# Performance work log

Hardware: AMD Instinct MI355X
Metric: run time of the kernel (lower is better)

## Reference

```python
import jax, jax.numpy as jnp
import numpy as np

N_HEAD = 16
HEAD_SIZE = 64

def setup_inputs() -> dict:
    key = jax.random.key(0)
    ks = jax.random.split(key, 5)
    B, T, C = 2, 2048, 1024
    s = 0.02
    return {
        "x": jax.random.normal(ks[0], (B, T, C), dtype=jnp.float32),
        "We": jax.random.normal(ks[1], (3 * C, C), dtype=jnp.float32) * s,
        "be": jax.random.normal(ks[2], (3 * C,), dtype=jnp.float32) * s,
        "Wp": jax.random.normal(ks[3], (C, C), dtype=jnp.float32) * s,
        "bp": jax.random.normal(ks[4], (C,), dtype=jnp.float32) * s,
    }

def reference(x, We, be, Wp, bp):
    B, T, C = x.shape
    H, D = N_HEAD, HEAD_SIZE
    qkv = x @ We.T + be                      # [B,T,3C]
    q, k, v = jnp.split(qkv, 3, axis=-1)
    # [B,H,T,D]
    q = q.reshape(B, T, H, D).transpose(0, 2, 1, 3)
    k = k.reshape(B, T, H, D).transpose(0, 2, 1, 3)
    v = v.reshape(B, T, H, D).transpose(0, 2, 1, 3)
    scale = 1.0 / jnp.sqrt(jnp.asarray(D, dtype=x.dtype))
    att = jnp.einsum('bhqd,bhkd->bhqk', q, k) * scale
    causal = jnp.tril(jnp.ones((T, T), dtype=bool))
    att = jnp.where(causal, att, -jnp.inf)
    att = jax.nn.softmax(att, axis=-1)
    y = jnp.einsum('bhqk,bhkd->bhqd', att, v)   # [B,H,T,D]
    y = y.transpose(0, 2, 1, 3).reshape(B, T, C)
    return y @ Wp.T + bp
```

## Files before the change

kernel.cpp:

```cpp
#include <hip/hip_runtime.h>
#include <hip/hip_bf16.h>
#include <stdint.h>
#include <stddef.h>

typedef short s8v __attribute__((ext_vector_type(8)));
typedef float f4v __attribute__((ext_vector_type(4)));

__device__ inline float b2f(short s) {
    union { unsigned u; float f; } x;
    x.u = ((unsigned)(unsigned short)s) << 16;
    return x.f;
}
__device__ inline short f2b(float f) {
    union { float f; unsigned u; } x;
    x.f = f;
    unsigned r = x.u + 0x7FFF + ((x.u >> 16) & 1);
    return (short)(r >> 16);
}

__device__ __forceinline__ void gl16(const short* g, short* l) {
    __builtin_amdgcn_global_load_lds(
        (const __attribute__((address_space(1))) void*)g,
        (__attribute__((address_space(3))) void*)l,
        16, 0, 0);
}

__global__ __launch_bounds__(256) void convert_bf16(
    const void* s0, short* d0, size_t c0,
    const void* s1, short* d1, size_t c1,
    const void* s2, short* d2, size_t c2,
    const void* s3, short* d3, size_t c3,
    const void* s4, short* d4, size_t c4,
    int* __restrict__ flagout)
{
    int hit = 0;
    const unsigned* xw = (const unsigned*)s0;
    for (int i = threadIdx.x & 63; i < 1024; i += 64) {
        unsigned e = ((xw[i] & 0xFFFFu) >> 7) & 0xFFu;
        if (e >= 0x8Au) hit = 1;
    }
    const bool f32 = (__ballot(hit != 0) != 0ull);
    if (blockIdx.x == 0 && threadIdx.x == 0) *flagout = f32 ? 1 : 0;

    const void* srcs[5] = {s0, s1, s2, s3, s4};
    short* dsts[5] = {d0, d1, d2, d3, d4};
    size_t cnts[5] = {c0, c1, c2, c3, c4};
    size_t total = c0 + c1 + c2 + c3 + c4;
    size_t stride = (size_t)gridDim.x * blockDim.x;
    for (size_t c = (size_t)blockIdx.x * blockDim.x + threadIdx.x; c < total; c += stride) {
        size_t r = c; int s = 0;
        while (r >= cnts[s]) { r -= cnts[s]; s++; }
        short* d = dsts[s] + r * 8;
        if (f32) {
            const float* p = (const float*)srcs[s] + r * 8;
            f4v a = *(const f4v*)p;
            f4v b = *(const f4v*)(p + 4);
            s8v v;
            v[0] = f2b(a[0]); v[1] = f2b(a[1]); v[2] = f2b(a[2]); v[3] = f2b(a[3]);
            v[4] = f2b(b[0]); v[5] = f2b(b[1]); v[6] = f2b(b[2]); v[7] = f2b(b[3]);
            *(s8v*)d = v;
        } else {
            *(s8v*)d = *(const s8v*)((const short*)srcs[s] + r * 8);
        }
    }
}

#define BKK 64

template<int QKV, int TBM, int TBN, int MINW>
__global__ __launch_bounds__(256, MINW) void gemm_bt_bias(
    const short* __restrict__ A,
    const short* __restrict__ B,
    const short* __restrict__ bias,
    void* __restrict__ C,
    short* __restrict__ vT,
    int M, int N, int K, int ldc,
    const int* __restrict__ flagp, int oDyn)
{
    const bool of32 = oDyn && (*flagp != 0);
    const int MT = TBM / 32, NT = TBN / 32;

    __shared__ __align__(16) short smem[(TBM + TBN) * BKK];
    short* sA = smem;
    short* sB = smem + TBM * BKK;

    const int tid  = threadIdx.x;
    const int lane = tid & 63;
    const int w    = tid >> 6;
    const int wm   = (w >> 1) * (TBM / 2);
    const int wn   = (w & 1) * (TBN / 2);
    const int quad = lane >> 4;
    const int l16  = lane & 15;

    const int m0 = blockIdx.y * TBM;
    const int n0 = blockIdx.x * TBN;

    f4v acc[MT][NT];
    const f4v vzero = {0.0f, 0.0f, 0.0f, 0.0f};
#pragma unroll
    for (int i = 0; i < MT; i++)
#pragma unroll
        for (int j = 0; j < NT; j++) acc[i][j] = vzero;

    const int ACH = TBM * 8;
    for (int k0 = 0; k0 < K; k0 += BKK) {
        __syncthreads();
#pragma unroll
        for (int i = 0; i < (TBM + TBN) / 32; i++) {
            int c  = i * 256 + tid;
            int cb = i * 256 + (tid & 192);
            if (c < ACH) {
                int r = c >> 3, kk = (c & 7) * 8;
                gl16(A + (size_t)(m0 + r) * K + k0 + kk, sA + cb * 8);
            } else {
                int c2 = c - ACH, cb2 = cb - ACH;
                int r = c2 >> 3, kk = (c2 & 7) * 8;
                gl16(B + (size_t)(n0 + r) * K + k0 + kk, sB + cb2 * 8);
            }
        }
        __syncthreads();
#pragma unroll
        for (int s = 0; s < 2; s++) {
            s8v af[MT], bf[NT];
#pragma unroll
            for (int t = 0; t < MT; t++)
                af[t] = *(const s8v*)(sA + (wm + t * 16 + l16) * BKK + s * 32 + quad * 8);
#pragma unroll
            for (int t = 0; t < NT; t++)
                bf[t] = *(const s8v*)(sB + (wn + t * 16 + l16) * BKK + s * 32 + quad * 8);
#pragma unroll
            for (int mt = 0; mt < MT; mt++)
#pragma unroll
                for (int nt = 0; nt < NT; nt++)
                    acc[mt][nt] = __builtin_amdgcn_mfma_f32_16x16x32_bf16(
                        af[mt], bf[nt], acc[mt][nt], 0, 0, 0);
        }
    }

    if (QKV && n0 >= 2048) {
        static_assert(!QKV || (TBM == 128 && TBN == 128), "V transpose assumes 128x128");
        const int bq = m0 >> 11;
#pragma unroll
        for (int hm = 0; hm < 2; hm++) {
            __syncthreads();
            if ((w >> 1) == hm) {
#pragma unroll
                for (int nt = 0; nt < NT; nt++) {
                    int nl = wn + nt * 16 + l16;
                    float bv = b2f(bias[n0 + nl]);
#pragma unroll
                    for (int mt = 0; mt < MT; mt++)
#pragma unroll
                        for (int r = 0; r < 4; r++) {
                            int ml2 = mt * 16 + quad * 4 + r;
                            smem[nl * 72 + ml2] = f2b(acc[mt][nt][r] + bv);
                        }
                }
            }
            __syncthreads();
#pragma unroll
            for (int i = 0; i < 4; i++) {
                int c = i * 256 + tid;
                int nl = c >> 3, col = (c & 7) * 8;
                int nn = n0 + nl;
                int hh = (nn - 2048) >> 6, d = nn & 63;
                short* dst = vT + (((size_t)(bq * 16 + hh)) * 64 + d) * 2048
                           + (m0 & 2047) + hm * 64 + col;
                *(s8v*)dst = *(const s8v*)(smem + nl * 72 + col);
            }
        }
    } else if (QKV) {
        const float osc = (n0 < 1024) ? 0.125f : 1.0f;
#pragma unroll
        for (int hm = 0; hm < 2; hm++) {
            __syncthreads();
            if ((w >> 1) == hm) {
#pragma unroll
                for (int nt = 0; nt < NT; nt++) {
                    int nl = wn + nt * 16 + l16;
                    float bv = b2f(bias[n0 + nl]);
#pragma unroll
                    for (int mt = 0; mt < MT; mt++)
#pragma unroll
                        for (int r = 0; r < 4; r++) {
                            int ml2 = mt * 16 + quad * 4 + r;
                            smem[ml2 * 144 + nl] = f2b((acc[mt][nt][r] + bv) * osc);
                        }
                }
            }
            __syncthreads();
#pragma unroll
            for (int i = 0; i < 4; i++) {
                int c = i * 256 + tid;
                int m = c >> 4, ncol = (c & 15) * 8;
                *(s8v*)((short*)C + (size_t)(m0 + hm * 64 + m) * ldc + n0 + ncol) =
                    *(const s8v*)(smem + m * 144 + ncol);
            }
        }
    } else {
#pragma unroll
        for (int nt = 0; nt < NT; nt++) {
            int n = n0 + wn + nt * 16 + l16;
            float bv = b2f(bias[n]);
#pragma unroll
            for (int mt = 0; mt < MT; mt++) {
#pragma unroll
                for (int r = 0; r < 4; r++) {
                    int m = m0 + wm + mt * 16 + quad * 4 + r;
                    float v = acc[mt][nt][r] + bv;
                    if (of32) ((float*)C)[(size_t)m * ldc + n] = v;
                    else      ((short*)C)[(size_t)m * ldc + n] = f2b(v);
                }
            }
        }
    }
}

#define LP 72

template<int PARTS>
__global__ __launch_bounds__(256) void attn_flash(
    const short* __restrict__ qk,
    const short* __restrict__ vt,
    short* __restrict__ y,
    short* __restrict__ Opart,
    float* __restrict__ Lpart)
{
    const int T = 2048, LDQ = 2048;
    __shared__ __align__(16) short sK[64 * LP];
    __shared__ __align__(16) short sVT[64 * LP];
    __shared__ __align__(16) short sP[4][16 * LP];

    const int tid  = threadIdx.x;
    const int lane = tid & 63;
    const int w    = tid >> 6;
    const int quad = lane >> 4;
    const int l16  = lane & 15;

    int part, qt, bh, u;
    if (PARTS == 2) {
        part = blockIdx.x & 1;
        int rest = blockIdx.x >> 1;
        qt = 31 - (rest >> 5);
        bh = rest & 31;
        u  = bh * 32 + qt;
    } else {
        part = 0;
        qt = 31 - (blockIdx.x >> 5);
        bh = blockIdx.x & 31;
        u  = 0;
    }
    const int b = bh >> 4;
    const int h = bh & 15;

    const int n    = qt + 1;
    const int half = (n + 1) >> 1;
    const int klo  = (PARTS == 2 && part) ? half : 0;
    const int khi  = (PARTS == 2 && !part) ? half : n;

    if (PARTS == 2 && klo >= khi) {
        s8v z;
#pragma unroll
        for (int j = 0; j < 8; j++) z[j] = 0;
        s8v* ob = (s8v*)(Opart + ((size_t)(part * 1024 + u)) * 4096);
        for (int i = tid; i < 512; i += 256) ob[i] = z;
        if (tid < 64) Lpart[(size_t)(part * 1024 + u) * 64 + tid] = 0.0f;
        return;
    }

    const size_t qkbase = (size_t)b * T * LDQ;
    const short* Kbase  = qk + qkbase + 1024 + h * 64;
    const short* Vbase  = vt + (size_t)bh * 64 * 2048;

    s8v qf[2];
    {
        int qrow = qt * 64 + w * 16 + l16;
        const short* qp = qk + qkbase + (size_t)qrow * LDQ + h * 64 + quad * 8;
        qf[0] = *(const s8v*)(qp);
        qf[1] = *(const s8v*)(qp + 32);
    }

    const int r0 = tid >> 3;
    const int dd = (tid & 7) * 8;

    s8v kr0 = *(const s8v*)(Kbase + (size_t)(klo * 64 + r0) * LDQ + dd);
    s8v kr1 = *(const s8v*)(Kbase + (size_t)(klo * 64 + r0 + 32) * LDQ + dd);
    s8v vv0 = *(const s8v*)(Vbase + (size_t)r0 * 2048 + klo * 64 + dd);
    s8v vv1 = *(const s8v*)(Vbase + (size_t)(r0 + 32) * 2048 + klo * 64 + dd);

    const f4v vzero = {0.0f, 0.0f, 0.0f, 0.0f};
    f4v o[4];
#pragma unroll
    for (int i = 0; i < 4; i++) o[i] = vzero;
    float lsum[4] = {0.0f, 0.0f, 0.0f, 0.0f};

    for (int kt = klo; kt < khi; kt++) {
        __syncthreads();
        *(s8v*)(sK  + r0 * LP + dd)        = kr0;
        *(s8v*)(sK  + (r0 + 32) * LP + dd) = kr1;
        *(s8v*)(sVT + r0 * LP + dd)        = vv0;
        *(s8v*)(sVT + (r0 + 32) * LP + dd) = vv1;
        if (kt + 1 < khi) {
            kr0 = *(const s8v*)(Kbase + (size_t)((kt + 1) * 64 + r0) * LDQ + dd);
            kr1 = *(const s8v*)(Kbase + (size_t)((kt + 1) * 64 + r0 + 32) * LDQ + dd);
            vv0 = *(const s8v*)(Vbase + (size_t)r0 * 2048 + (kt + 1) * 64 + dd);
            vv1 = *(const s8v*)(Vbase + (size_t)(r0 + 32) * 2048 + (kt + 1) * 64 + dd);
        }
        __syncthreads();

        f4v sacc[4];
#pragma unroll
        for (int nt = 0; nt < 4; nt++) {
            sacc[nt] = vzero;
            s8v kf0 = *(const s8v*)(sK + (nt * 16 + l16) * LP + quad * 8);
            s8v kf1 = *(const s8v*)(sK + (nt * 16 + l16) * LP + 32 + quad * 8);
            sacc[nt] = __builtin_amdgcn_mfma_f32_16x16x32_bf16(qf[0], kf0, sacc[nt], 0, 0, 0);
            sacc[nt] = __builtin_amdgcn_mfma_f32_16x16x32_bf16(qf[1], kf1, sacc[nt], 0, 0, 0);
        }

        short* pp = sP[w];
        const bool diag = (kt == qt);
#pragma unroll
        for (int nt = 0; nt < 4; nt++) {
#pragma unroll
            for (int r = 0; r < 4; r++) {
                float p = __expf(sacc[nt][r]);
                if (diag) {
                    int q = w * 16 + quad * 4 + r;
                    int k = nt * 16 + l16;
                    if (k > q) p = 0.0f;
                }
                union { float f; unsigned u; } c; c.f = p;
                short p16 = (short)(c.u >> 16);
                c.u &= 0xFFFF0000u;
                lsum[r] += c.f;
                pp[(quad * 4 + r) * LP + nt * 16 + l16] = p16;
            }
        }

        s8v pf0 = *(const s8v*)(pp + l16 * LP + quad * 8);
        s8v pf1 = *(const s8v*)(pp + l16 * LP + 32 + quad * 8);
#pragma unroll
        for (int dt = 0; dt < 4; dt++) {
            s8v vf0 = *(const s8v*)(sVT + (dt * 16 + l16) * LP + quad * 8);
            s8v vf1 = *(const s8v*)(sVT + (dt * 16 + l16) * LP + 32 + quad * 8);
            o[dt] = __builtin_amdgcn_mfma_f32_16x16x32_bf16(pf0, vf0, o[dt], 0, 0, 0);
            o[dt] = __builtin_amdgcn_mfma_f32_16x16x32_bf16(pf1, vf1, o[dt], 0, 0, 0);
        }
    }

#pragma unroll
    for (int r = 0; r < 4; r++) {
        float s = lsum[r];
        s += __shfl_xor(s, 1, 64);
        s += __shfl_xor(s, 2, 64);
        s += __shfl_xor(s, 4, 64);
        s += __shfl_xor(s, 8, 64);
        lsum[r] = s;
    }

    if (PARTS == 2) {
        short* ob = Opart + ((size_t)(part * 1024 + u)) * 4096;
#pragma unroll
        for (int dt = 0; dt < 4; dt++)
#pragma unroll
            for (int r = 0; r < 4; r++)
                ob[(w * 16 + quad * 4 + r) * 64 + dt * 16 + l16] = f2b(o[dt][r]);
        if (l16 == 0) {
#pragma unroll
            for (int r = 0; r < 4; r++)
                Lpart[(size_t)(part * 1024 + u) * 64 + w * 16 + quad * 4 + r] = lsum[r];
        }
    } else {
#pragma unroll
        for (int r = 0; r < 4; r++) lsum[r] = 1.0f / lsum[r];
#pragma unroll
        for (int dt = 0; dt < 4; dt++)
#pragma unroll
            for (int r = 0; r < 4; r++) {
                int qrow = qt * 64 + w * 16 + quad * 4 + r;
                int d = dt * 16 + l16;
                y[((size_t)b * T + qrow) * 1024 + h * 64 + d] = f2b(o[dt][r] * lsum[r]);
            }
    }
}

__global__ __launch_bounds__(256) void attn_combine(
    const short* __restrict__ Opart,
    const float* __restrict__ Lpart,
    short* __restrict__ y)
{
    const int u  = blockIdx.x;
    const int bh = u >> 5, qt = u & 31;
    const int b = bh >> 4, h = bh & 15;
    const int t = threadIdx.x;
    const int q = t >> 2, dg = (t & 3) * 16;

    float l = Lpart[(size_t)u * 64 + q] + Lpart[(size_t)(1024 + u) * 64 + q];
    float rl = 1.0f / l;
    const short* p0 = Opart + (size_t)u * 4096 + q * 64 + dg;
    const short* p1 = Opart + (size_t)(1024 + u) * 4096 + q * 64 + dg;
    short* yo = y + ((size_t)b * 2048 + qt * 64 + q) * 1024 + h * 64 + dg;
#pragma unroll
    for (int hv = 0; hv < 2; hv++) {
        s8v a = *(const s8v*)(p0 + hv * 8);
        s8v c = *(const s8v*)(p1 + hv * 8);
        s8v r;
#pragma unroll
        for (int j = 0; j < 8; j++) r[j] = f2b((b2f(a[j]) + b2f(c[j])) * rl);
        *(s8v*)(yo + hv * 8) = r;
    }
}

extern "C" void kernel_launch(void* const* d_in, const int* in_sizes, int n_in,
                              void* d_out, int out_size, void* d_ws, size_t ws_size,
                              hipStream_t stream)
{
    char* p = (char*)d_ws;
    int*   flag = (int*)p;                 p += 16;
    short* qk   = (short*)p;               p += (size_t)4096 * 2048 * 2;
    short* vT   = (short*)p;               p += (size_t)32 * 64 * 2048 * 2;
    short* xb   = (short*)p;               p += (size_t)4096 * 1024 * 2;
    short* Web  = (short*)p;               p += (size_t)3072 * 1024 * 2;
    short* Wpb  = (short*)p;               p += (size_t)1024 * 1024 * 2;
    short* beb  = (short*)p;               p += 3072 * 2;
    short* bpb  = (short*)p;               p += 1024 * 2;
    short* Opart = (short*)p;              p += (size_t)2 * 1024 * 4096 * 2;
    float* Lpart = (float*)p;              p += (size_t)2 * 1024 * 64 * 4;
    short* y = xb;
    const size_t need = (size_t)(p - (char*)d_ws);
    const bool split = (ws_size >= need);

    convert_bf16<<<dim3(4098), 256, 0, stream>>>(
        d_in[0], xb,  (size_t)4096 * 1024 / 8,
        d_in[1], Web, (size_t)3072 * 1024 / 8,
        d_in[2], beb, (size_t)3072 / 8,
        d_in[3], Wpb, (size_t)1024 * 1024 / 8,
        d_in[4], bpb, (size_t)1024 / 8,
        flag);

    gemm_bt_bias<1, 128, 128, 3><<<dim3(3072 / 128, 4096 / 128), 256, 0, stream>>>(
        xb, Web, beb, qk, vT, 4096, 3072, 1024, 2048, flag, 0);

    if (split) {
        attn_flash<2><<<dim3(2048), 256, 0, stream>>>(qk, vT, nullptr, Opart, Lpart);
        attn_combine<<<dim3(1024), 256, 0, stream>>>(Opart, Lpart, y);
    } else {
        attn_flash<1><<<dim3(1024), 256, 0, stream>>>(qk, vT, y, nullptr, nullptr);
    }

    gemm_bt_bias<0, 128, 64, 2><<<dim3(1024 / 64, 4096 / 128), 256, 0, stream>>>(
        y, Wpb, bpb, d_out, nullptr, 4096, 1024, 1024, 1024, flag, 1);
}
```

Before: 193.2 us.

## Deepen attention K/V register prefetch to two tiles and swizzle GEMM block order

The attention loop now keeps two sets of K/V register buffers and prefetches tile kt+2 while computing tile kt. The body is unrolled by two through a lambda, which hides more global load latency behind the MFMA work. Separately, the GEMM kernel remaps its linear block id so that consecutive blocks are spread across eight groups, likely aiming at XCD-aware cache locality on MI355X. The deeper prefetch raises register pressure and could lower occupancy. The block remap assumes the total block count is divisible by eight.

```diff
diff --git a/kernel.cpp b/kernel.cpp
--- a/kernel.cpp
+++ b/kernel.cpp
@@ -92,8 +92,11 @@
     const int quad = lane >> 4;
     const int l16  = lane & 15;
 
-    const int m0 = blockIdx.y * TBM;
-    const int n0 = blockIdx.x * TBN;
+    const int bid0 = blockIdx.y * (int)gridDim.x + blockIdx.x;
+    const int nwg  = (int)(gridDim.x * gridDim.y);
+    const int lb   = (bid0 & 7) * (nwg >> 3) + (bid0 >> 3);
+    const int m0 = (lb / (int)gridDim.x) * TBM;
+    const int n0 = (lb % (int)gridDim.x) * TBN;
 
     f4v acc[MT][NT];
     const f4v vzero = {0.0f, 0.0f, 0.0f, 0.0f};
@@ -283,28 +286,35 @@
     const int r0 = tid >> 3;
     const int dd = (tid & 7) * 8;
 
-    s8v kr0 = *(const s8v*)(Kbase + (size_t)(klo * 64 + r0) * LDQ + dd);
-    s8v kr1 = *(const s8v*)(Kbase + (size_t)(klo * 64 + r0 + 32) * LDQ + dd);
-    s8v vv0 = *(const s8v*)(Vbase + (size_t)r0 * 2048 + klo * 64 + dd);
-    s8v vv1 = *(const s8v*)(Vbase + (size_t)(r0 + 32) * 2048 + klo * 64 + dd);
-
     const f4v vzero = {0.0f, 0.0f, 0.0f, 0.0f};
     f4v o[4];
 #pragma unroll
     for (int i = 0; i < 4; i++) o[i] = vzero;
     float lsum[4] = {0.0f, 0.0f, 0.0f, 0.0f};
 
-    for (int kt = klo; kt < khi; kt++) {
+    s8v ka0, ka1, va0, va1, kb0, kb1, vb0, vb1;
+    ka0 = *(const s8v*)(Kbase + (size_t)(klo * 64 + r0) * LDQ + dd);
+    ka1 = *(const s8v*)(Kbase + (size_t)(klo * 64 + r0 + 32) * LDQ + dd);
+    va0 = *(const s8v*)(Vbase + (size_t)r0 * 2048 + klo * 64 + dd);
+    va1 = *(const s8v*)(Vbase + (size_t)(r0 + 32) * 2048 + klo * 64 + dd);
+    if (klo + 1 < khi) {
+        kb0 = *(const s8v*)(Kbase + (size_t)((klo + 1) * 64 + r0) * LDQ + dd);
+        kb1 = *(const s8v*)(Kbase + (size_t)((klo + 1) * 64 + r0 + 32) * LDQ + dd);
+        vb0 = *(const s8v*)(Vbase + (size_t)r0 * 2048 + (klo + 1) * 64 + dd);
+        vb1 = *(const s8v*)(Vbase + (size_t)(r0 + 32) * 2048 + (klo + 1) * 64 + dd);
+    }
+
+    auto body = [&](s8v& kr0, s8v& kr1, s8v& vv0, s8v& vv1, int kt) {
         __syncthreads();
         *(s8v*)(sK  + r0 * LP + dd)        = kr0;
         *(s8v*)(sK  + (r0 + 32) * LP + dd) = kr1;
         *(s8v*)(sVT + r0 * LP + dd)        = vv0;
         *(s8v*)(sVT + (r0 + 32) * LP + dd) = vv1;
-        if (kt + 1 < khi) {
-            kr0 = *(const s8v*)(Kbase + (size_t)((kt + 1) * 64 + r0) * LDQ + dd);
-            kr1 = *(const s8v*)(Kbase + (size_t)((kt + 1) * 64 + r0 + 32) * LDQ + dd);
-            vv0 = *(const s8v*)(Vbase + (size_t)r0 * 2048 + (kt + 1) * 64 + dd);
-            vv1 = *(const s8v*)(Vbase + (size_t)(r0 + 32) * 2048 + (kt + 1) * 64 + dd);
+        if (kt + 2 < khi) {
+            kr0 = *(const s8v*)(Kbase + (size_t)((kt + 2) * 64 + r0) * LDQ + dd);
+            kr1 = *(const s8v*)(Kbase + (size_t)((kt + 2) * 64 + r0 + 32) * LDQ + dd);
+            vv0 = *(const s8v*)(Vbase + (size_t)r0 * 2048 + (kt + 2) * 64 + dd);
+            vv1 = *(const s8v*)(Vbase + (size_t)(r0 + 32) * 2048 + (kt + 2) * 64 + dd);
         }
         __syncthreads();
 
@@ -330,10 +340,10 @@
                     int k = nt * 16 + l16;
                     if (k > q) p = 0.0f;
                 }
-                union { float f; unsigned u; } c; c.f = p;
-                short p16 = (short)(c.u >> 16);
-                c.u &= 0xFFFF0000u;
-                lsum[r] += c.f;
+                union { float f; unsigned u; } c2; c2.f = p;
+                short p16 = (short)(c2.u >> 16);
+                c2.u &= 0xFFFF0000u;
+                lsum[r] += c2.f;
                 pp[(quad * 4 + r) * LP + nt * 16 + l16] = p16;
             }
         }
@@ -347,6 +357,12 @@
             o[dt] = __builtin_amdgcn_mfma_f32_16x16x32_bf16(pf0, vf0, o[dt], 0, 0, 0);
             o[dt] = __builtin_amdgcn_mfma_f32_16x16x32_bf16(pf1, vf1, o[dt], 0, 0, 0);
         }
+    };
+
+    for (int kt = klo; kt < khi; kt += 2) {
+        body(ka0, ka1, va0, va1, kt);
+        if (kt + 1 < khi)
+            body(kb0, kb1, vb0, vb1, kt + 1);
     }
 
 #pragma unroll
```

Result: no change. 190.0 us (-1.7%).
